# Kernel optimization log

Measured on AMD Instinct MI355X. Metric: run time of the kernel, lower is better.

The kernel has to match this reference:

```python
import jax, jax.numpy as jnp
import numpy as np

D_MODEL = 1024
MEM_SIZE = 131072
TOP_K = 64
D_STATE = 16
D_CONV = 4
D_INNER = 2 * D_MODEL          # expand=2
DT_RANK = (D_MODEL + 15) // 16  # ceil(d_model/16) = 64
EPS_COS = 1e-8
EPS_LN = 1e-5


def setup_inputs() -> dict:
    key = jax.random.key(0)
    ks = jax.random.split(key, 12)
    s = 0.02
    inp = {
        "query": jax.random.normal(ks[0], (D_MODEL,), jnp.float32),
        "memory": jax.random.normal(ks[1], (MEM_SIZE, D_MODEL), jnp.float32),
        "memory_usage": jnp.zeros((MEM_SIZE,), jnp.int32),
        # Mamba block params
        "in_proj_w": jax.random.normal(ks[2], (2 * D_INNER, D_MODEL), jnp.float32) * s,
        "conv_w": jax.random.normal(ks[3], (D_INNER, D_CONV), jnp.float32) * s,
        "conv_b": jnp.zeros((D_INNER,), jnp.float32),
        "x_proj_w": jax.random.normal(ks[4], (DT_RANK + 2 * D_STATE, D_INNER), jnp.float32) * s,
        "dt_proj_w": jax.random.normal(ks[5], (D_INNER, DT_RANK), jnp.float32) * s,
        "dt_proj_b": jax.random.normal(ks[6], (D_INNER,), jnp.float32) * s,
        "A_log": jnp.log(jnp.broadcast_to(jnp.arange(1, D_STATE + 1, dtype=jnp.float32), (D_INNER, D_STATE))),
        "D": jnp.ones((D_INNER,), jnp.float32),
        "out_proj_w": jax.random.normal(ks[7], (D_MODEL, D_INNER), jnp.float32) * s,
        # LayerNorm params
        "ln_g": jnp.ones((D_MODEL,), jnp.float32),
        "ln_b": jnp.zeros((D_MODEL,), jnp.float32),
    }
    return inp


def _mamba(x, in_proj_w, conv_w, conv_b, x_proj_w, dt_proj_w, dt_proj_b, A_log, D, out_proj_w):
    # x: (B, L, d_model)
    B, L, _ = x.shape
    xz = jnp.einsum("bld,ed->ble", x, in_proj_w)            # (B, L, 2*d_inner)
    u, z = jnp.split(xz, 2, axis=-1)                          # each (B, L, d_inner)
    # depthwise causal conv1d, kernel D_CONV
    up = jnp.pad(u, ((0, 0), (D_CONV - 1, 0), (0, 0)))
    uc = sum(up[:, j:j + L, :] * conv_w[:, j] for j in range(D_CONV)) + conv_b
    u = jax.nn.silu(uc)
    x_dbl = jnp.einsum("bld,ed->ble", u, x_proj_w)           # (B, L, dt_rank+2*d_state)
    dt = x_dbl[..., :DT_RANK]
    Bm = x_dbl[..., DT_RANK:DT_RANK + D_STATE]               # (B, L, d_state)
    Cm = x_dbl[..., DT_RANK + D_STATE:]                      # (B, L, d_state)
    delta = jax.nn.softplus(jnp.einsum("blr,dr->bld", dt, dt_proj_w) + dt_proj_b)  # (B, L, d_inner)
    A = -jnp.exp(A_log)                                       # (d_inner, d_state)
    deltaA = jnp.exp(delta[..., None] * A)                    # (B, L, d_inner, d_state)
    dBu = delta[..., None] * Bm[:, :, None, :] * u[..., None]

    def step(h, inputs):
        dA_t, dBu_t, C_t = inputs                             # (B,d,s),(B,d,s),(B,s)
        h = dA_t * h + dBu_t
        y = jnp.einsum("bds,bs->bd", h, C_t)
        return h, y

    h0 = jnp.zeros((B, D_INNER, D_STATE), x.dtype)
    xs = (jnp.swapaxes(deltaA, 0, 1), jnp.swapaxes(dBu, 0, 1), jnp.swapaxes(Cm, 0, 1))
    _, ys = jax.lax.scan(step, h0, xs)                        # (L, B, d_inner)
    y = jnp.swapaxes(ys, 0, 1) + u * D
    y = y * jax.nn.silu(z)
    return jnp.einsum("bld,ed->ble", y, out_proj_w)          # (B, L, d_model)


def reference(query, memory, memory_usage, in_proj_w, conv_w, conv_b, x_proj_w,
              dt_proj_w, dt_proj_b, A_log, D, out_proj_w, ln_g, ln_b):
    # cosine similarity of query vs every memory row (torch eps semantics)
    dots = memory @ query                                     # (MEM,)
    denom = jnp.maximum(jnp.linalg.norm(memory, axis=1) * jnp.linalg.norm(query), EPS_COS)
    sims = dots / denom
    _, idx = jax.lax.top_k(sims, TOP_K)
    retrieved = memory[idx]                                   # (k, d_model)
    usage_new = memory_usage.at[idx].add(1)
    seq = retrieved[None]                                     # (1, k, d_model)
    processed = _mamba(seq, in_proj_w, conv_w, conv_b, x_proj_w,
                       dt_proj_w, dt_proj_b, A_log, D, out_proj_w)
    ctx = processed[:, -1, :]                                 # (1, d_model)
    mu = jnp.mean(ctx, axis=-1, keepdims=True)
    var = jnp.var(ctx, axis=-1, keepdims=True)
    out = (ctx - mu) * jax.lax.rsqrt(var + EPS_LN) * ln_g + ln_b
    return out, usage_new
```

## Files before the change

### kernel.cpp

```cpp
#include <hip/hip_runtime.h>
#include <math.h>

#define D_MODEL   1024
#define MEM_SIZE  131072
#define TOP_K     64
#define D_STATE   16
#define D_CONV    4
#define D_INNER   2048
#define DT_RANK   64

#define WS_CAND1   0u
#define WS_CAND2   262144u
#define WS_CAND3   278528u
#define WS_IDXF    279552u
#define WS_U       294912u
#define WS_US      819200u
#define WS_XDBL    1343488u
#define WS_DELTA   1368064u
#define WS_Z63     1892352u
#define WS_YFIN    1900544u
#define WS_CTX     1908736u

typedef float vfloat4 __attribute__((ext_vector_type(4)));

__device__ __forceinline__ float wave_reduce_add(float v) {
#pragma unroll
  for (int off = 32; off > 0; off >>= 1) v += __shfl_xor(v, off, 64);
  return v;
}

__device__ __forceinline__ vfloat4 ld_nt(const float* p) {
  return __builtin_nontemporal_load((const vfloat4*)p);
}

__device__ __forceinline__ unsigned long long pack_key(float sim, int idx) {
  unsigned int fb = __float_as_uint(sim);
  fb = (fb & 0x80000000u) ? ~fb : (fb | 0x80000000u);
  return ((unsigned long long)fb << 32) | (unsigned int)(~(unsigned int)idx);
}

template <int N>
__device__ __forceinline__ void bitonic_sort_desc(unsigned long long* keys, int tid) {
  for (int k = 2; k <= N; k <<= 1) {
    for (int j = k >> 1; j > 0; j >>= 1) {
      for (int i = tid; i < N; i += 256) {
        int ixj = i ^ j;
        if (ixj > i) {
          unsigned long long a = keys[i], b = keys[ixj];
          bool desc = ((i & k) == 0);
          if (desc ? (a < b) : (a > b)) { keys[i] = b; keys[ixj] = a; }
        }
      }
      __syncthreads();
    }
  }
}

__global__ __launch_bounds__(256) void k_sims(const float* __restrict__ mem,
                                              const float* __restrict__ query,
                                              const int* __restrict__ usage_in,
                                              float* __restrict__ usage_out,
                                              unsigned long long* __restrict__ cand1) {
  __shared__ float red[4];
  __shared__ unsigned long long keys[256];
  const int tid = threadIdx.x, lane = tid & 63, wave = tid >> 6;

  {
    const int gi = blockIdx.x * 256 + tid;
    usage_out[gi] = (float)usage_in[gi];
  }

  const float4* q4 = (const float4*)query;
  float4 qf[4];
  float qs = 0.f;
#pragma unroll
  for (int c = 0; c < 4; ++c) {
    qf[c] = q4[c * 64 + lane];
    qs += qf[c].x * qf[c].x + qf[c].y * qf[c].y + qf[c].z * qf[c].z + qf[c].w * qf[c].w;
  }
  qs = wave_reduce_add(qs);
  if (lane == 0) red[wave] = qs;
  __syncthreads();
  const float qn = sqrtf(red[0] + red[1] + red[2] + red[3]);

  const int base = blockIdx.x * 256 + wave * 64;
  for (int it = 0; it < 16; ++it) {
    const int r0 = base + it * 4;
    float d[4] = {0.f, 0.f, 0.f, 0.f}, s[4] = {0.f, 0.f, 0.f, 0.f};
#pragma unroll
    for (int c = 0; c < 4; ++c) {
#pragma unroll
      for (int k = 0; k < 4; ++k) {
        vfloat4 a = ld_nt(mem + (size_t)(r0 + k) * 1024 + c * 256 + lane * 4);
        d[k] += a.x * qf[c].x + a.y * qf[c].y + a.z * qf[c].z + a.w * qf[c].w;
        s[k] += a.x * a.x + a.y * a.y + a.z * a.z + a.w * a.w;
      }
    }
#pragma unroll
    for (int k = 0; k < 4; ++k) {
      d[k] = wave_reduce_add(d[k]);
      s[k] = wave_reduce_add(s[k]);
    }
    if (lane == 0) {
#pragma unroll
      for (int k = 0; k < 4; ++k) {
        float sim = d[k] / fmaxf(sqrtf(s[k]) * qn, 1e-8f);
        keys[wave * 64 + it * 4 + k] = pack_key(sim, r0 + k);
      }
    }
  }
  __syncthreads();
  bitonic_sort_desc<256>(keys, tid);
  if (tid < 64) cand1[blockIdx.x * 64 + tid] = keys[tid];
}

__global__ __launch_bounds__(256) void k_merge16(const unsigned long long* __restrict__ in,
                                                 unsigned long long* __restrict__ outk) {
  __shared__ unsigned long long keys[1024];
  const int tid = threadIdx.x;
  for (int i = tid; i < 1024; i += 256) keys[i] = in[blockIdx.x * 1024 + i];
  __syncthreads();
  bitonic_sort_desc<1024>(keys, tid);
  if (tid < 64) outk[blockIdx.x * 64 + tid] = keys[tid];
}

__global__ __launch_bounds__(256) void k_final(const unsigned long long* __restrict__ in,
                                               int* __restrict__ idxf,
                                               float* __restrict__ usage_out) {
  __shared__ unsigned long long keys[128];
  const int tid = threadIdx.x;
  if (tid < 128) keys[tid] = in[tid];
  __syncthreads();
  bitonic_sort_desc<128>(keys, tid);
  if (tid < 64) {
    unsigned int low = (unsigned int)(keys[tid] & 0xFFFFFFFFull);
    int idx = (int)(~low);
    idxf[tid] = idx;
    usage_out[idx] += 1.0f;
  }
}

__global__ __launch_bounds__(256) void k_inproj(const float* __restrict__ mem,
                                                const float* __restrict__ inw,
                                                const int* __restrict__ idxf,
                                                float* __restrict__ u,
                                                float* __restrict__ z63) {
  const int tid = threadIdx.x, lane = tid & 63, wave = tid >> 6;
  const int bid = blockIdx.x;
  const float4* m4 = (const float4*)mem;
  const float4* w4 = (const float4*)inw;
  if (bid < 256) {
    const int e0 = bid * 8 + wave * 2;
    float4 wa[4], wb[4];
#pragma unroll
    for (int c = 0; c < 4; ++c) {
      wa[c] = w4[e0 * 256 + c * 64 + lane];
      wb[c] = w4[(e0 + 1) * 256 + c * 64 + lane];
    }
    for (int l = 0; l < 64; ++l) {
      const int r = idxf[l];
      float da = 0.f, db = 0.f;
#pragma unroll
      for (int c = 0; c < 4; ++c) {
        float4 x = m4[r * 256 + c * 64 + lane];
        da += x.x * wa[c].x + x.y * wa[c].y + x.z * wa[c].z + x.w * wa[c].w;
        db += x.x * wb[c].x + x.y * wb[c].y + x.z * wb[c].z + x.w * wb[c].w;
      }
      da = wave_reduce_add(da);
      db = wave_reduce_add(db);
      if (lane == 0) {
        u[l * 2048 + e0]     = da;
        u[l * 2048 + e0 + 1] = db;
      }
    }
  } else {
    const int wid = (bid - 256) * 4 + wave;
    const int r63 = idxf[63];
    float4 xf[4];
#pragma unroll
    for (int c = 0; c < 4; ++c) xf[c] = m4[r63 * 256 + c * 64 + lane];
    for (int j = 0; j < 16; ++j) {
      const int e = 2048 + wid * 16 + j;
      float dsum = 0.f;
#pragma unroll
      for (int c = 0; c < 4; ++c) {
        float4 w = w4[e * 256 + c * 64 + lane];
        dsum += w.x * xf[c].x + w.y * xf[c].y + w.z * xf[c].z + w.w * xf[c].w;
      }
      dsum = wave_reduce_add(dsum);
      if (lane == 0) z63[e - 2048] = dsum;
    }
  }
}

__global__ __launch_bounds__(256) void k_conv(const float* __restrict__ u,
                                              const float* __restrict__ cw,
                                              const float* __restrict__ cb,
                                              float* __restrict__ us) {
  const int e = blockIdx.x * 256 + threadIdx.x;
  const int l = blockIdx.y;
  float acc = cb[e];
#pragma unroll
  for (int j = 0; j < 4; ++j) {
    const int li = l - 3 + j;
    if (li >= 0) acc += u[li * 2048 + e] * cw[e * 4 + j];
  }
  us[l * 2048 + e] = acc / (1.f + __expf(-acc));
}

__global__ __launch_bounds__(256) void k_xproj(const float* __restrict__ us,
                                               const float* __restrict__ xw,
                                               float* __restrict__ xdbl) {
  __shared__ __align__(16) float su[2048];
  const int tid = threadIdx.x, lane = tid & 63, wave = tid >> 6;
  const int l = blockIdx.x;
  for (int i = tid; i < 2048; i += 256) su[i] = us[l * 2048 + i];
  __syncthreads();
  const float4* su4 = (const float4*)su;
  const float4* xw4 = (const float4*)xw;
  for (int j = wave; j < 96; j += 4) {
    float dsum = 0.f;
#pragma unroll
    for (int c = 0; c < 8; ++c) {
      float4 a = su4[c * 64 + lane];
      float4 w = xw4[j * 512 + c * 64 + lane];
      dsum += a.x * w.x + a.y * w.y + a.z * w.z + a.w * w.w;
    }
    dsum = wave_reduce_add(dsum);
    if (lane == 0) xdbl[l * 96 + j] = dsum;
  }
}

__global__ __launch_bounds__(256) void k_dtproj(const float* __restrict__ xdbl,
                                                const float* __restrict__ dtw,
                                                const float* __restrict__ dtb,
                                                float* __restrict__ delta) {
  const int d = blockIdx.x * 256 + threadIdx.x;
  const int l0 = blockIdx.y * 8;
  float w[64];
  const float4* dtw4 = (const float4*)dtw;
#pragma unroll
  for (int c = 0; c < 16; ++c) {
    float4 t = dtw4[d * 16 + c];
    w[c * 4] = t.x; w[c * 4 + 1] = t.y; w[c * 4 + 2] = t.z; w[c * 4 + 3] = t.w;
  }
  const float b = dtb[d];
  for (int l = 0; l < 8; ++l) {
    float acc = b;
    const float* arow = xdbl + (l0 + l) * 96;
#pragma unroll
    for (int r = 0; r < 64; ++r) acc += w[r] * arow[r];
    float sp = fmaxf(acc, 0.f) + log1pf(__expf(-fabsf(acc)));
    delta[(l0 + l) * 2048 + d] = sp;
  }
}

__global__ __launch_bounds__(256) void k_scan(const float* __restrict__ delta,
                                              const float* __restrict__ us,
                                              const float* __restrict__ xdbl,
                                              const float* __restrict__ A_log,
                                              const float* __restrict__ Dp,
                                              const float* __restrict__ z63,
                                              float* __restrict__ yfin) {
  const int t = blockIdx.x * 256 + threadIdx.x;
  const int d = t >> 4, s = t & 15;
  const float A = -__expf(A_log[t]);
  float h = 0.f;
#pragma unroll 8
  for (int l = 0; l < 64; ++l) {
    float dl = delta[l * 2048 + d];
    float ul = us[l * 2048 + d];
    float bl = xdbl[l * 96 + 64 + s];
    h = __expf(dl * A) * h + dl * bl * ul;
  }
  float v = h * xdbl[63 * 96 + 80 + s];
#pragma unroll
  for (int off = 8; off >= 1; off >>= 1) v += __shfl_xor(v, off, 64);
  if (s == 0) {
    float y = v + us[63 * 2048 + d] * Dp[d];
    float z = z63[d];
    yfin[d] = y * (z / (1.f + __expf(-z)));
  }
}

__global__ __launch_bounds__(256) void k_outproj(const float* __restrict__ yfin,
                                                 const float* __restrict__ ow,
                                                 float* __restrict__ ctx) {
  const int tid = threadIdx.x, lane = tid & 63, wave = tid >> 6;
  const int m = blockIdx.x * 4 + wave;
  const float4* y4 = (const float4*)yfin;
  const float4* ow4 = (const float4*)ow;
  float dsum = 0.f;
#pragma unroll
  for (int c = 0; c < 8; ++c) {
    float4 w = ow4[m * 512 + c * 64 + lane];
    float4 y = y4[c * 64 + lane];
    dsum += w.x * y.x + w.y * y.y + w.z * y.z + w.w * y.w;
  }
  dsum = wave_reduce_add(dsum);
  if (lane == 0) ctx[m] = dsum;
}

__global__ __launch_bounds__(256) void k_ln(const float* __restrict__ ctx,
                                            const float* __restrict__ g,
                                            const float* __restrict__ b,
                                            float* __restrict__ out) {
  __shared__ float red[8];
  const int tid = threadIdx.x, lane = tid & 63, wave = tid >> 6;
  float4 v = ((const float4*)ctx)[tid];
  float s1 = v.x + v.y + v.z + v.w;
  float s2 = v.x * v.x + v.y * v.y + v.z * v.z + v.w * v.w;
  s1 = wave_reduce_add(s1);
  s2 = wave_reduce_add(s2);
  if (lane == 0) { red[wave] = s1; red[4 + wave] = s2; }
  __syncthreads();
  const float mu = (red[0] + red[1] + red[2] + red[3]) * (1.f / 1024.f);
  const float var = (red[4] + red[5] + red[6] + red[7]) * (1.f / 1024.f) - mu * mu;
  const float rs = rsqrtf(var + 1e-5f);
  const int i0 = tid * 4;
  out[i0 + 0] = (v.x - mu) * rs * g[i0 + 0] + b[i0 + 0];
  out[i0 + 1] = (v.y - mu) * rs * g[i0 + 1] + b[i0 + 1];
  out[i0 + 2] = (v.z - mu) * rs * g[i0 + 2] + b[i0 + 2];
  out[i0 + 3] = (v.w - mu) * rs * g[i0 + 3] + b[i0 + 3];
}

extern "C" void kernel_launch(void* const* d_in, const int* in_sizes, int n_in,
                              void* d_out, int out_size, void* d_ws, size_t ws_size,
                              hipStream_t stream) {
  const float* query    = (const float*)d_in[0];
  const float* memory   = (const float*)d_in[1];
  const int*   usage_in = (const int*)d_in[2];
  const float* in_proj  = (const float*)d_in[3];
  const float* conv_w   = (const float*)d_in[4];
  const float* conv_b   = (const float*)d_in[5];
  const float* x_proj   = (const float*)d_in[6];
  const float* dt_proj  = (const float*)d_in[7];
  const float* dt_bias  = (const float*)d_in[8];
  const float* A_log    = (const float*)d_in[9];
  const float* Dp       = (const float*)d_in[10];
  const float* out_proj = (const float*)d_in[11];
  const float* ln_g     = (const float*)d_in[12];
  const float* ln_b     = (const float*)d_in[13];

  char* ws = (char*)d_ws;
  unsigned long long* cand1 = (unsigned long long*)(ws + WS_CAND1);
  unsigned long long* cand2 = (unsigned long long*)(ws + WS_CAND2);
  unsigned long long* cand3 = (unsigned long long*)(ws + WS_CAND3);
  int*   idxf  = (int*)(ws + WS_IDXF);
  float* u     = (float*)(ws + WS_U);
  float* us_   = (float*)(ws + WS_US);
  float* xdbl  = (float*)(ws + WS_XDBL);
  float* delta = (float*)(ws + WS_DELTA);
  float* z63   = (float*)(ws + WS_Z63);
  float* yfin  = (float*)(ws + WS_YFIN);
  float* ctx   = (float*)(ws + WS_CTX);

  float* out_ln    = (float*)d_out;
  float* usage_out = (float*)d_out + 1024;

  hipLaunchKernelGGL(k_sims,    dim3(512), dim3(256), 0, stream, memory, query, usage_in, usage_out, cand1);
  hipLaunchKernelGGL(k_merge16, dim3(32),  dim3(256), 0, stream, cand1, cand2);
  hipLaunchKernelGGL(k_merge16, dim3(2),   dim3(256), 0, stream, cand2, cand3);
  hipLaunchKernelGGL(k_final,   dim3(1),   dim3(256), 0, stream, cand3, idxf, usage_out);
  hipLaunchKernelGGL(k_inproj,  dim3(288), dim3(256), 0, stream, memory, in_proj, idxf, u, z63);
  hipLaunchKernelGGL(k_conv,    dim3(8, 64), dim3(256), 0, stream, u, conv_w, conv_b, us_);
  hipLaunchKernelGGL(k_xproj,   dim3(64),  dim3(256), 0, stream, us_, x_proj, xdbl);
  hipLaunchKernelGGL(k_dtproj,  dim3(8, 8), dim3(256), 0, stream, xdbl, dt_proj, dt_bias, delta);
  hipLaunchKernelGGL(k_scan,    dim3(128), dim3(256), 0, stream, delta, us_, xdbl, A_log, Dp, z63, yfin);
  hipLaunchKernelGGL(k_outproj, dim3(256), dim3(256), 0, stream, yfin, out_proj, ctx);
  hipLaunchKernelGGL(k_ln,      dim3(1),   dim3(256), 0, stream, ctx, ln_g, ln_b, out_ln);
}
```

Before: 898.5 us.

## Fuse conv into x_proj and dt_proj into scan, restructure top-k merge

The similarity pass now uses 1024 blocks of 128 rows, with plain loads in place of nontemporal loads. The top-k reduction changes from three merge levels to two larger 2048-key bitonic sorts. The depthwise conv plus SiLU is folded into the x_proj kernel, and the dt_proj plus softplus is computed in shared memory inside the scan kernel, which removes two launches and the delta buffer round trip. The cost is larger serial bitonic sorts in the final single-block stage and recomputed xdbl staging per scan block.

```diff
diff --git a/kernel.cpp b/kernel.cpp
--- a/kernel.cpp
+++ b/kernel.cpp
@@ -10,27 +10,19 @@
 #define DT_RANK   64
 
 #define WS_CAND1   0u
-#define WS_CAND2   262144u
-#define WS_CAND3   278528u
-#define WS_IDXF    279552u
-#define WS_U       294912u
-#define WS_US      819200u
-#define WS_XDBL    1343488u
-#define WS_DELTA   1368064u
-#define WS_Z63     1892352u
-#define WS_YFIN    1900544u
-#define WS_CTX     1908736u
-
-typedef float vfloat4 __attribute__((ext_vector_type(4)));
+#define WS_CAND2   524288u
+#define WS_IDXF    540672u
+#define WS_U       540928u
+#define WS_US      1065216u
+#define WS_XDBL    1589504u
+#define WS_Z63     1614080u
+#define WS_YFIN    1622272u
+#define WS_CTX     1630464u
 
 __device__ __forceinline__ float wave_reduce_add(float v) {
 #pragma unroll
   for (int off = 32; off > 0; off >>= 1) v += __shfl_xor(v, off, 64);
   return v;
-}
-
-__device__ __forceinline__ vfloat4 ld_nt(const float* p) {
-  return __builtin_nontemporal_load((const vfloat4*)p);
 }
 
 __device__ __forceinline__ unsigned long long pack_key(float sim, int idx) {
@@ -61,16 +53,17 @@
                                               const int* __restrict__ usage_in,
                                               float* __restrict__ usage_out,
                                               unsigned long long* __restrict__ cand1) {
-  __shared__ float red[4];
-  __shared__ unsigned long long keys[256];
-  const int tid = threadIdx.x, lane = tid & 63, wave = tid >> 6;
-
-  {
-    const int gi = blockIdx.x * 256 + tid;
+  __shared__ float redq;
+  __shared__ unsigned long long keys[128];
+  const int tid = threadIdx.x, lane = tid & 63, wave = tid >> 6;
+
+  if (tid < 128) {
+    const int gi = blockIdx.x * 128 + tid;
     usage_out[gi] = (float)usage_in[gi];
   }
 
   const float4* q4 = (const float4*)query;
+  const float4* m4 = (const float4*)mem;
   float4 qf[4];
   float qs = 0.f;
 #pragma unroll
@@ -79,19 +72,19 @@
     qs += qf[c].x * qf[c].x + qf[c].y * qf[c].y + qf[c].z * qf[c].z + qf[c].w * qf[c].w;
   }
   qs = wave_reduce_add(qs);
-  if (lane == 0) red[wave] = qs;
-  __syncthreads();
-  const float qn = sqrtf(red[0] + red[1] + red[2] + red[3]);
-
-  const int base = blockIdx.x * 256 + wave * 64;
-  for (int it = 0; it < 16; ++it) {
+  if (tid == 0) redq = qs;
+  __syncthreads();
+  const float qn = sqrtf(redq);
+
+  const int base = blockIdx.x * 128 + wave * 32;
+  for (int it = 0; it < 8; ++it) {
     const int r0 = base + it * 4;
     float d[4] = {0.f, 0.f, 0.f, 0.f}, s[4] = {0.f, 0.f, 0.f, 0.f};
 #pragma unroll
     for (int c = 0; c < 4; ++c) {
 #pragma unroll
       for (int k = 0; k < 4; ++k) {
-        vfloat4 a = ld_nt(mem + (size_t)(r0 + k) * 1024 + c * 256 + lane * 4);
+        float4 a = m4[(size_t)(r0 + k) * 256 + c * 64 + lane];
         d[k] += a.x * qf[c].x + a.y * qf[c].y + a.z * qf[c].z + a.w * qf[c].w;
         s[k] += a.x * a.x + a.y * a.y + a.z * a.z + a.w * a.w;
       }
@@ -105,33 +98,33 @@
 #pragma unroll
       for (int k = 0; k < 4; ++k) {
         float sim = d[k] / fmaxf(sqrtf(s[k]) * qn, 1e-8f);
-        keys[wave * 64 + it * 4 + k] = pack_key(sim, r0 + k);
-      }
-    }
-  }
-  __syncthreads();
-  bitonic_sort_desc<256>(keys, tid);
+        keys[wave * 32 + it * 4 + k] = pack_key(sim, r0 + k);
+      }
+    }
+  }
+  __syncthreads();
+  bitonic_sort_desc<128>(keys, tid);
   if (tid < 64) cand1[blockIdx.x * 64 + tid] = keys[tid];
 }
 
-__global__ __launch_bounds__(256) void k_merge16(const unsigned long long* __restrict__ in,
-                                                 unsigned long long* __restrict__ outk) {
-  __shared__ unsigned long long keys[1024];
+__global__ __launch_bounds__(256) void k_merge2048(const unsigned long long* __restrict__ in,
+                                                   unsigned long long* __restrict__ outk) {
+  __shared__ unsigned long long keys[2048];
   const int tid = threadIdx.x;
-  for (int i = tid; i < 1024; i += 256) keys[i] = in[blockIdx.x * 1024 + i];
-  __syncthreads();
-  bitonic_sort_desc<1024>(keys, tid);
+  for (int i = tid; i < 2048; i += 256) keys[i] = in[blockIdx.x * 2048 + i];
+  __syncthreads();
+  bitonic_sort_desc<2048>(keys, tid);
   if (tid < 64) outk[blockIdx.x * 64 + tid] = keys[tid];
 }
 
-__global__ __launch_bounds__(256) void k_final(const unsigned long long* __restrict__ in,
-                                               int* __restrict__ idxf,
-                                               float* __restrict__ usage_out) {
-  __shared__ unsigned long long keys[128];
+__global__ __launch_bounds__(256) void k_final2048(const unsigned long long* __restrict__ in,
+                                                   int* __restrict__ idxf,
+                                                   float* __restrict__ usage_out) {
+  __shared__ unsigned long long keys[2048];
   const int tid = threadIdx.x;
-  if (tid < 128) keys[tid] = in[tid];
-  __syncthreads();
-  bitonic_sort_desc<128>(keys, tid);
+  for (int i = tid; i < 2048; i += 256) keys[i] = in[i];
+  __syncthreads();
+  bitonic_sort_desc<2048>(keys, tid);
   if (tid < 64) {
     unsigned int low = (unsigned int)(keys[tid] & 0xFFFFFFFFull);
     int idx = (int)(~low);
@@ -162,7 +155,7 @@
       float da = 0.f, db = 0.f;
 #pragma unroll
       for (int c = 0; c < 4; ++c) {
-        float4 x = m4[r * 256 + c * 64 + lane];
+        float4 x = m4[(size_t)r * 256 + c * 64 + lane];
         da += x.x * wa[c].x + x.y * wa[c].y + x.z * wa[c].z + x.w * wa[c].w;
         db += x.x * wb[c].x + x.y * wb[c].y + x.z * wb[c].z + x.w * wb[c].w;
       }
@@ -178,7 +171,7 @@
     const int r63 = idxf[63];
     float4 xf[4];
 #pragma unroll
-    for (int c = 0; c < 4; ++c) xf[c] = m4[r63 * 256 + c * 64 + lane];
+    for (int c = 0; c < 4; ++c) xf[c] = m4[(size_t)r63 * 256 + c * 64 + lane];
     for (int j = 0; j < 16; ++j) {
       const int e = 2048 + wid * 16 + j;
       float dsum = 0.f;
@@ -193,28 +186,31 @@
   }
 }
 
-__global__ __launch_bounds__(256) void k_conv(const float* __restrict__ u,
-                                              const float* __restrict__ cw,
-                                              const float* __restrict__ cb,
-                                              float* __restrict__ us) {
-  const int e = blockIdx.x * 256 + threadIdx.x;
-  const int l = blockIdx.y;
-  float acc = cb[e];
-#pragma unroll
-  for (int j = 0; j < 4; ++j) {
-    const int li = l - 3 + j;
-    if (li >= 0) acc += u[li * 2048 + e] * cw[e * 4 + j];
-  }
-  us[l * 2048 + e] = acc / (1.f + __expf(-acc));
-}
-
-__global__ __launch_bounds__(256) void k_xproj(const float* __restrict__ us,
-                                               const float* __restrict__ xw,
-                                               float* __restrict__ xdbl) {
+__global__ __launch_bounds__(256) void k_xprojc(const float* __restrict__ u,
+                                                const float* __restrict__ cw,
+                                                const float* __restrict__ cb,
+                                                const float* __restrict__ xw,
+                                                float* __restrict__ us,
+                                                float* __restrict__ xdbl) {
   __shared__ __align__(16) float su[2048];
   const int tid = threadIdx.x, lane = tid & 63, wave = tid >> 6;
   const int l = blockIdx.x;
-  for (int i = tid; i < 2048; i += 256) su[i] = us[l * 2048 + i];
+  for (int i = tid; i < 2048; i += 256) {
+    float acc = cb[i];
+    const float4 w = ((const float4*)cw)[i];
+    if (l >= 3) {
+      acc += u[(l - 3) * 2048 + i] * w.x + u[(l - 2) * 2048 + i] * w.y +
+             u[(l - 1) * 2048 + i] * w.z + u[l * 2048 + i] * w.w;
+    } else {
+      if (l - 3 + 1 >= 0) acc += u[(l - 2) * 2048 + i] * w.y;
+      if (l - 3 + 2 >= 0) acc += u[(l - 1) * 2048 + i] * w.z;
+      acc += u[l * 2048 + i] * w.w;
+      if (l == 2) acc += u[0] * 0.f;
+    }
+    const float sv = acc / (1.f + __expf(-acc));
+    su[i] = sv;
+    us[l * 2048 + i] = sv;
+  }
   __syncthreads();
   const float4* su4 = (const float4*)su;
   const float4* xw4 = (const float4*)xw;
@@ -231,54 +227,61 @@
   }
 }
 
-__global__ __launch_bounds__(256) void k_dtproj(const float* __restrict__ xdbl,
-                                                const float* __restrict__ dtw,
-                                                const float* __restrict__ dtb,
-                                                float* __restrict__ delta) {
-  const int d = blockIdx.x * 256 + threadIdx.x;
-  const int l0 = blockIdx.y * 8;
-  float w[64];
-  const float4* dtw4 = (const float4*)dtw;
-#pragma unroll
-  for (int c = 0; c < 16; ++c) {
-    float4 t = dtw4[d * 16 + c];
-    w[c * 4] = t.x; w[c * 4 + 1] = t.y; w[c * 4 + 2] = t.z; w[c * 4 + 3] = t.w;
-  }
-  const float b = dtb[d];
-  for (int l = 0; l < 8; ++l) {
-    float acc = b;
-    const float* arow = xdbl + (l0 + l) * 96;
-#pragma unroll
-    for (int r = 0; r < 64; ++r) acc += w[r] * arow[r];
-    float sp = fmaxf(acc, 0.f) + log1pf(__expf(-fabsf(acc)));
-    delta[(l0 + l) * 2048 + d] = sp;
-  }
-}
-
-__global__ __launch_bounds__(256) void k_scan(const float* __restrict__ delta,
-                                              const float* __restrict__ us,
-                                              const float* __restrict__ xdbl,
-                                              const float* __restrict__ A_log,
-                                              const float* __restrict__ Dp,
-                                              const float* __restrict__ z63,
-                                              float* __restrict__ yfin) {
-  const int t = blockIdx.x * 256 + threadIdx.x;
-  const int d = t >> 4, s = t & 15;
-  const float A = -__expf(A_log[t]);
+__global__ __launch_bounds__(256) void k_scanf(const float* __restrict__ xdbl,
+                                               const float* __restrict__ dtw,
+                                               const float* __restrict__ dtb,
+                                               const float* __restrict__ us,
+                                               const float* __restrict__ A_log,
+                                               const float* __restrict__ Dp,
+                                               const float* __restrict__ z63,
+                                               float* __restrict__ yfin) {
+  __shared__ float xl[64 * 97];
+  __shared__ float wl[16 * 65];
+  __shared__ float dl[64 * 17];
+  __shared__ float ul[64 * 17];
+  const int tid = threadIdx.x;
+  const int d0 = blockIdx.x * 16;
+
+  for (int i = tid; i < 6144; i += 256) {
+    const int l = i / 96, r = i - l * 96;
+    xl[l * 97 + r] = xdbl[i];
+  }
+  for (int i = tid; i < 1024; i += 256) {
+    const int dd = i >> 6, r = i & 63;
+    wl[dd * 65 + r] = dtw[(d0 + dd) * 64 + r];
+  }
+  for (int i = tid; i < 1024; i += 256) {
+    const int l = i >> 4, dd = i & 15;
+    ul[l * 17 + dd] = us[l * 2048 + d0 + dd];
+  }
+  __syncthreads();
+
+  for (int i = tid; i < 1024; i += 256) {
+    const int l = i >> 4, dd = i & 15;
+    float acc = dtb[d0 + dd];
+#pragma unroll
+    for (int r = 0; r < 64; ++r) acc += xl[l * 97 + r] * wl[dd * 65 + r];
+    dl[l * 17 + dd] = fmaxf(acc, 0.f) + log1pf(__expf(-fabsf(acc)));
+  }
+  __syncthreads();
+
+  const int dd = tid >> 4, s = tid & 15;
+  const int d = d0 + dd;
+  const float A = -__expf(A_log[d * 16 + s]);
   float h = 0.f;
 #pragma unroll 8
   for (int l = 0; l < 64; ++l) {
-    float dl = delta[l * 2048 + d];
-    float ul = us[l * 2048 + d];
-    float bl = xdbl[l * 96 + 64 + s];
-    h = __expf(dl * A) * h + dl * bl * ul;
-  }
-  float v = h * xdbl[63 * 96 + 80 + s];
+    const float dlv = dl[l * 17 + dd];
+    const float bl  = xl[l * 97 + 64 + s];
+    const float uv  = ul[l * 17 + dd];
+    h = __expf(dlv * A) * h + dlv * bl * uv;
+  }
+  float v = h * xl[63 * 97 + 80 + s];
 #pragma unroll
   for (int off = 8; off >= 1; off >>= 1) v += __shfl_xor(v, off, 64);
   if (s == 0) {
-    float y = v + us[63 * 2048 + d] * Dp[d];
-    float z = z63[d];
+    const float y = v + ul[63 * 17 + dd] * Dp[d];
+    const float z = z63[d];
     yfin[d] = y * (z / (1.f + __expf(-z)));
   }
 }
@@ -345,12 +348,10 @@
   char* ws = (char*)d_ws;
   unsigned long long* cand1 = (unsigned long long*)(ws + WS_CAND1);
   unsigned long long* cand2 = (unsigned long long*)(ws + WS_CAND2);
-  unsigned long long* cand3 = (unsigned long long*)(ws + WS_CAND3);
   int*   idxf  = (int*)(ws + WS_IDXF);
   float* u     = (float*)(ws + WS_U);
   float* us_   = (float*)(ws + WS_US);
   float* xdbl  = (float*)(ws + WS_XDBL);
-  float* delta = (float*)(ws + WS_DELTA);
   float* z63   = (float*)(ws + WS_Z63);
   float* yfin  = (float*)(ws + WS_YFIN);
   float* ctx   = (float*)(ws + WS_CTX);
@@ -358,15 +359,12 @@
   float* out_ln    = (float*)d_out;
   float* usage_out = (float*)d_out + 1024;
 
-  hipLaunchKernelGGL(k_sims,    dim3(512), dim3(256), 0, stream, memory, query, usage_in, usage_out, cand1);
-  hipLaunchKernelGGL(k_merge16, dim3(32),  dim3(256), 0, stream, cand1, cand2);
-  hipLaunchKernelGGL(k_merge16, dim3(2),   dim3(256), 0, stream, cand2, cand3);
-  hipLaunchKernelGGL(k_final,   dim3(1),   dim3(256), 0, stream, cand3, idxf, usage_out);
-  hipLaunchKernelGGL(k_inproj,  dim3(288), dim3(256), 0, stream, memory, in_proj, idxf, u, z63);
-  hipLaunchKernelGGL(k_conv,    dim3(8, 64), dim3(256), 0, stream, u, conv_w, conv_b, us_);
-  hipLaunchKernelGGL(k_xproj,   dim3(64),  dim3(256), 0, stream, us_, x_proj, xdbl);
-  hipLaunchKernelGGL(k_dtproj,  dim3(8, 8), dim3(256), 0, stream, xdbl, dt_proj, dt_bias, delta);
-  hipLaunchKernelGGL(k_scan,    dim3(128), dim3(256), 0, stream, delta, us_, xdbl, A_log, Dp, z63, yfin);
-  hipLaunchKernelGGL(k_outproj, dim3(256), dim3(256), 0, stream, yfin, out_proj, ctx);
-  hipLaunchKernelGGL(k_ln,      dim3(1),   dim3(256), 0, stream, ctx, ln_g, ln_b, out_ln);
-}
+  hipLaunchKernelGGL(k_sims,      dim3(1024), dim3(256), 0, stream, memory, query, usage_in, usage_out, cand1);
+  hipLaunchKernelGGL(k_merge2048, dim3(32),   dim3(256), 0, stream, cand1, cand2);
+  hipLaunchKernelGGL(k_final2048, dim3(1),    dim3(256), 0, stream, cand2, idxf, usage_out);
+  hipLaunchKernelGGL(k_inproj,    dim3(288),  dim3(256), 0, stream, memory, in_proj, idxf, u, z63);
+  hipLaunchKernelGGL(k_xprojc,    dim3(64),   dim3(256), 0, stream, u, conv_w, conv_b, x_proj, us_, xdbl);
+  hipLaunchKernelGGL(k_scanf,     dim3(128),  dim3(256), 0, stream, xdbl, dt_proj, dt_bias, us_, A_log, Dp, z63, yfin);
+  hipLaunchKernelGGL(k_outproj,   dim3(256),  dim3(256), 0, stream, yfin, out_proj, ctx);
+  hipLaunchKernelGGL(k_ln,        dim3(1),    dim3(256), 0, stream, ctx, ln_g, ln_b, out_ln);
+}
```

New measurement: 998.0 us. +11.1%, slower.
